# Kernel optimization log

Measured on AMD Instinct MI355X. Metric: run time of the kernel, lower is better.

The kernel has to match this reference:

```python
import jax, jax.numpy as jnp
import numpy as np

N, D, H = 8192, 256, 128


def setup_inputs() -> dict:
    key = jax.random.key(0)
    k1, k2, k3, k4 = jax.random.split(key, 4)
    x = jax.random.normal(k1, (N, D), dtype=jnp.float32)
    y = jax.random.normal(k2, (N, D), dtype=jnp.float32)
    W1 = jax.random.normal(k3, (D, H), dtype=jnp.float32) * (1.0 / np.sqrt(D))
    b1 = jnp.zeros((H,), dtype=jnp.float32)
    W2 = jax.random.normal(k4, (H, D), dtype=jnp.float32) * (1.0 / np.sqrt(H))
    b2 = jnp.zeros((D,), dtype=jnp.float32)
    return {"x": x, "y": y, "W1": W1, "b1": b1, "W2": W2, "b2": b2}


def _l2norm(v):
    # torch.nn.functional.normalize(dim=-1): v / max(||v||, eps)
    n = jnp.sqrt(jnp.sum(v * v, axis=-1, keepdims=True))
    return v / jnp.maximum(n, 1e-12)


def _neg_cos_loss_stopgrad(p, z):
    p_n = _l2norm(p)
    z_n = _l2norm(jax.lax.stop_gradient(z))
    return -jnp.mean(jnp.sum(p_n * z_n, axis=1))


def reference(x, y, W1, b1, W2, b2):
    def mlp(v):
        h = jax.nn.relu(v @ W1 + b1)
        return h @ W2 + b2

    p_x = mlp(x)
    p_y = mlp(y)
    loss = 0.5 * (_neg_cos_loss_stopgrad(p_x, y) + _neg_cos_loss_stopgrad(p_y, x))

    # accuracy branch (original naively broadcasts [N,D,1]*[1,D,N]; same math as matmul)
    p_x_n = _l2norm(p_x)
    p_y_n = _l2norm(p_y)
    x_n = _l2norm(x)
    y_n = _l2norm(y)
    sim_x = p_x_n @ y_n.T  # [N, N], sim_x[i, j] = p_x[i] . y[j]
    sim_y = p_y_n @ x_n.T  # [N, N]
    gold = jnp.arange(x.shape[0])
    # NOTE: faithful to original parenthesization: 0.5 * first term + second term
    acc_x = 0.5 * jnp.mean((jnp.argmax(sim_x, axis=0) == gold).astype(jnp.float32)) + \
            jnp.mean((jnp.argmax(sim_x, axis=1) == gold).astype(jnp.float32))
    acc_y = 0.5 * jnp.mean((jnp.argmax(sim_y, axis=0) == gold).astype(jnp.float32)) + \
            jnp.mean((jnp.argmax(sim_y, axis=1) == gold).astype(jnp.float32))
    return loss, acc_x, acc_y
```

## Files before the change

### kernel.cpp

```cpp
#include <hip/hip_runtime.h>


static constexpr int N = 8192;
static constexpr int D = 256;
static constexpr int H = 128;

typedef __attribute__((ext_vector_type(8))) short s16x8;
typedef __attribute__((ext_vector_type(4))) float fp32x4;
typedef unsigned long long ull;

__device__ __forceinline__ unsigned f2ord(float f) {
    unsigned u = __float_as_uint(f);
    return (u & 0x80000000u) ? ~u : (u | 0x80000000u);
}
__device__ __forceinline__ ull umax64(ull a, ull b) { return a > b ? a : b; }
__device__ __forceinline__ unsigned short bf16_rtne(float f) {
    unsigned u = __float_as_uint(f);
    unsigned r = 0x7FFFu + ((u >> 16) & 1u);
    return (unsigned short)((u + r) >> 16);
}
__device__ __forceinline__ float bf_f(unsigned short h) {
    return __uint_as_float((unsigned)h << 16);
}
__device__ __forceinline__ void split_store(float f, unsigned short* h, unsigned short* l) {
    unsigned short hb = bf16_rtne(f);
    *h = hb;
    *l = bf16_rtne(f - bf_f(hb));
}
__device__ __forceinline__ void gload16(const unsigned short* g, void* lds) {
    __builtin_amdgcn_global_load_lds(
        (const __attribute__((address_space(1))) unsigned int*)g,
        (__attribute__((address_space(3))) unsigned int*)lds, 16, 0, 0);
}
__device__ __forceinline__ size_t gidx(int panel, int kt, int kq, int m) {
    return (((size_t)(panel * 8 + kt) * 4 + kq) * 128 + m) * 8;
}

static constexpr int MLP_ROWS = 32;

__global__ __launch_bounds__(256) void prep_kernel(
    const float* __restrict__ x, const float* __restrict__ y,
    const float* __restrict__ W1, const float* __restrict__ b1,
    const float* __restrict__ W2, const float* __restrict__ b2,
    unsigned short* __restrict__ pxh, unsigned short* __restrict__ pxl,
    unsigned short* __restrict__ pyh, unsigned short* __restrict__ pyl,
    unsigned short* __restrict__ xh, unsigned short* __restrict__ xl,
    unsigned short* __restrict__ yh, unsigned short* __restrict__ yl,
    ull* __restrict__ keys, int* __restrict__ cnt, float* __restrict__ diagParts)
{
    const int bid = blockIdx.x;
    const int t = threadIdx.x;

    if (bid < 512) {
        __shared__ float sV[MLP_ROWS][D + 4];
        __shared__ float sH[MLP_ROWS][H + 4];
        __shared__ float sNrm[MLP_ROWS];

        const float* V = (bid < 256) ? x : y;
        unsigned short* Ph = (bid < 256) ? pxh : pyh;
        unsigned short* Pl = (bid < 256) ? pxl : pyl;
        const int rowBase = (bid & 255) * MLP_ROWS;

        for (int i = t; i < MLP_ROWS * (D / 4); i += 256) {
            int r = i >> 6, c4 = i & 63;
            float4 v = *reinterpret_cast<const float4*>(&V[(size_t)(rowBase + r) * D + c4 * 4]);
            sV[r][c4 * 4 + 0] = v.x; sV[r][c4 * 4 + 1] = v.y;
            sV[r][c4 * 4 + 2] = v.z; sV[r][c4 * 4 + 3] = v.w;
        }
        __syncthreads();

        {
            const int c = t & (H - 1);
            const int r0 = (t >> 7) * 16;
            float acc[16];
#pragma unroll
            for (int i = 0; i < 16; ++i) acc[i] = 0.f;
            for (int k4 = 0; k4 < D / 4; ++k4) {
                float w0 = W1[(k4 * 4 + 0) * H + c];
                float w1 = W1[(k4 * 4 + 1) * H + c];
                float w2 = W1[(k4 * 4 + 2) * H + c];
                float w3 = W1[(k4 * 4 + 3) * H + c];
#pragma unroll
                for (int i = 0; i < 16; ++i) {
                    float4 v = *reinterpret_cast<const float4*>(&sV[r0 + i][k4 * 4]);
                    acc[i] = fmaf(v.w, w3, fmaf(v.z, w2, fmaf(v.y, w1, fmaf(v.x, w0, acc[i]))));
                }
            }
            float bb = b1[c];
#pragma unroll
            for (int i = 0; i < 16; ++i) {
                float h = acc[i] + bb;
                sH[r0 + i][c] = h > 0.f ? h : 0.f;
            }
        }
        __syncthreads();

        {
            const int c = t;
            float acc[MLP_ROWS];
#pragma unroll
            for (int i = 0; i < MLP_ROWS; ++i) acc[i] = 0.f;
            for (int k4 = 0; k4 < H / 4; ++k4) {
                float w0 = W2[(k4 * 4 + 0) * D + c];
                float w1 = W2[(k4 * 4 + 1) * D + c];
                float w2 = W2[(k4 * 4 + 2) * D + c];
                float w3 = W2[(k4 * 4 + 3) * D + c];
#pragma unroll
                for (int i = 0; i < MLP_ROWS; ++i) {
                    float4 v = *reinterpret_cast<const float4*>(&sH[i][k4 * 4]);
                    acc[i] = fmaf(v.w, w3, fmaf(v.z, w2, fmaf(v.y, w1, fmaf(v.x, w0, acc[i]))));
                }
            }
            float bb = b2[c];
            __syncthreads();
#pragma unroll
            for (int i = 0; i < MLP_ROWS; ++i) sV[i][c] = acc[i] + bb;
        }
        __syncthreads();

        {
            const int wave = t >> 6, lane = t & 63;
            for (int r = wave; r < MLP_ROWS; r += 4) {
                float s = 0.f;
#pragma unroll
                for (int c = 0; c < D / 64; ++c) {
                    float v = sV[r][lane + c * 64];
                    s = fmaf(v, v, s);
                }
#pragma unroll
                for (int off = 32; off > 0; off >>= 1) s += __shfl_down(s, off);
                if (lane == 0) sNrm[r] = s;
            }
        }
        __syncthreads();

        for (int i = t; i < MLP_ROWS * (D / 4); i += 256) {
            int r = i >> 6, c4 = i & 63;
            float scale = 1.0f / fmaxf(sqrtf(sNrm[r]), 1e-12f);
            ushort4 h, l;
            split_store(sV[r][c4 * 4 + 0] * scale, &h.x, &l.x);
            split_store(sV[r][c4 * 4 + 1] * scale, &h.y, &l.y);
            split_store(sV[r][c4 * 4 + 2] * scale, &h.z, &l.z);
            split_store(sV[r][c4 * 4 + 3] * scale, &h.w, &l.w);
            int grow = rowBase + r;
            size_t g = gidx(grow >> 7, c4 >> 3, (c4 >> 1) & 3, grow & 127) + (size_t)(c4 & 1) * 4;
            *reinterpret_cast<ushort4*>(&Ph[g]) = h;
            *reinterpret_cast<ushort4*>(&Pl[g]) = l;
        }
    } else {
        const int rb = bid - 512;
        if (t < 128) keys[rb * 128 + t] = 0ULL;
        if (bid == 512) {
            if (t < 128) diagParts[t] = 0.f;
            if (t < 4) cnt[t] = 0;
        }
        const int wave = t >> 6, lane = t & 63;
#pragma unroll 1
        for (int i = 0; i < 16; ++i) {
            int gr = rb * 64 + wave * 16 + i;
            const float* V = (gr < N) ? x : y;
            unsigned short* Vh = (gr < N) ? xh : yh;
            unsigned short* Vl = (gr < N) ? xl : yl;
            int row = gr & (N - 1);
            float4 v = *reinterpret_cast<const float4*>(&V[(size_t)row * D + lane * 4]);
            float s = fmaf(v.x, v.x, fmaf(v.y, v.y, fmaf(v.z, v.z, v.w * v.w)));
#pragma unroll
            for (int off = 32; off > 0; off >>= 1) s += __shfl_down(s, off);
            s = __shfl(s, 0);
            float scale = 1.0f / fmaxf(sqrtf(s), 1e-12f);
            ushort4 h, l;
            split_store(v.x * scale, &h.x, &l.x);
            split_store(v.y * scale, &h.y, &l.y);
            split_store(v.z * scale, &h.z, &l.z);
            split_store(v.w * scale, &h.w, &l.w);
            size_t g = gidx(row >> 7, lane >> 3, (lane >> 1) & 3, row & 127) + (size_t)(lane & 1) * 4;
            *reinterpret_cast<ushort4*>(&Vh[g]) = h;
            *reinterpret_cast<ushort4*>(&Vl[g]) = l;
        }
    }
}

__global__ __launch_bounds__(256, 4) void sim_argmax_mfma(
    const unsigned short* __restrict__ Ah, const unsigned short* __restrict__ Al,
    const unsigned short* __restrict__ Bh, const unsigned short* __restrict__ Bl,
    ull* __restrict__ rowKeys, ull* __restrict__ colKeys,
    float* __restrict__ diagParts)
{
    __shared__ s16x8 sS[4][512];
    __shared__ ull kbufR[128][2];
    __shared__ ull kbufC[128][2];
    __shared__ float sDiag[4];

    const int t = threadIdx.x;
    const int w = t >> 6, lane = t & 63;
    const int wr = w >> 1, wc = w & 1;

    const int bid = blockIdx.x;
    const int xcd = bid & 7, local = bid >> 3;
    const int rowTile = (xcd & 3) * 16 + (local & 15);
    const int colTile = (xcd >> 2) * 32 + (local >> 4);
    const int rowBase = rowTile * 128;
    const int colBase = colTile * 128;

    fp32x4 acc[4][4];
#pragma unroll
    for (int i = 0; i < 4; ++i)
#pragma unroll
        for (int j = 0; j < 4; ++j) acc[i][j] = (fp32x4){0.f, 0.f, 0.f, 0.f};

    const unsigned short* pAh = Ah + (size_t)rowTile * 4096 * 8;
    const unsigned short* pAl = Al + (size_t)rowTile * 4096 * 8;
    const unsigned short* pBh = Bh + (size_t)colTile * 4096 * 8;
    const unsigned short* pBl = Bl + (size_t)colTile * 4096 * 8;

#define STAGE(kt)                                                               \
    do {                                                                        \
        const size_t o0 = (size_t)(kt) * 512 + w * 128 + lane;                  \
        const size_t o1 = o0 + 64;                                              \
        gload16(pAh + o0 * 8, (void*)&sS[0][w * 128]);                          \
        gload16(pAh + o1 * 8, (void*)&sS[0][w * 128 + 64]);                     \
        gload16(pAl + o0 * 8, (void*)&sS[1][w * 128]);                          \
        gload16(pAl + o1 * 8, (void*)&sS[1][w * 128 + 64]);                     \
        gload16(pBh + o0 * 8, (void*)&sS[2][w * 128]);                          \
        gload16(pBh + o1 * 8, (void*)&sS[2][w * 128 + 64]);                     \
        gload16(pBl + o0 * 8, (void*)&sS[3][w * 128]);                          \
        gload16(pBl + o1 * 8, (void*)&sS[3][w * 128 + 64]);                     \
    } while (0)

    STAGE(0);

    const int fBase = (lane >> 4) * 128 + (lane & 15);
    const int aBase = fBase + wr * 64;
    const int bBase = fBase + wc * 64;

#pragma unroll 1
    for (int kt = 0; kt < 8; ++kt) {
        __syncthreads();

        s16x8 ah[4], bh[4];
#pragma unroll
        for (int f = 0; f < 4; ++f) ah[f] = sS[0][aBase + f * 16];
#pragma unroll
        for (int f = 0; f < 4; ++f) bh[f] = sS[2][bBase + f * 16];
        __builtin_amdgcn_s_setprio(1);
#pragma unroll
        for (int fm = 0; fm < 4; ++fm)
#pragma unroll
            for (int fn = 0; fn < 4; ++fn)
                acc[fm][fn] = __builtin_amdgcn_mfma_f32_16x16x32_bf16(ah[fm], bh[fn], acc[fm][fn], 0, 0, 0);
        __builtin_amdgcn_s_setprio(0);

        {
            s16x8 al[4];
#pragma unroll
            for (int f = 0; f < 4; ++f) al[f] = sS[1][aBase + f * 16];
            __builtin_amdgcn_s_setprio(1);
#pragma unroll
            for (int fm = 0; fm < 4; ++fm)
#pragma unroll
                for (int fn = 0; fn < 4; ++fn)
                    acc[fm][fn] = __builtin_amdgcn_mfma_f32_16x16x32_bf16(al[fm], bh[fn], acc[fm][fn], 0, 0, 0);
            __builtin_amdgcn_s_setprio(0);
        }

        {
            s16x8 bl[4];
#pragma unroll
            for (int f = 0; f < 4; ++f) bl[f] = sS[3][bBase + f * 16];

            __syncthreads();
            if (kt < 7) STAGE(kt + 1);

            __builtin_amdgcn_s_setprio(1);
#pragma unroll
            for (int fm = 0; fm < 4; ++fm)
#pragma unroll
                for (int fn = 0; fn < 4; ++fn)
                    acc[fm][fn] = __builtin_amdgcn_mfma_f32_16x16x32_bf16(ah[fm], bl[fn], acc[fm][fn], 0, 0, 0);
            __builtin_amdgcn_s_setprio(0);
        }
    }
#undef STAGE

    const int R0 = wr * 64;
    const int C0 = wc * 64;

    if (rowTile == colTile) {
        float s = 0.f;
        if (wr == wc) {
            int dr = (lane & 15) - (lane >> 4) * 4;
            if (dr >= 0 && dr < 4) {
#pragma unroll
                for (int fm = 0; fm < 4; ++fm) s += acc[fm][fm][dr];
            }
        }
#pragma unroll
        for (int off = 32; off > 0; off >>= 1) s += __shfl_down(s, off);
        if (lane == 0) sDiag[w] = s;
        __syncthreads();
        if (t == 0) diagParts[rowTile] = ((sDiag[0] + sDiag[1]) + sDiag[2]) + sDiag[3];
    }

#pragma unroll
    for (int fm = 0; fm < 4; ++fm) {
#pragma unroll
        for (int r = 0; r < 4; ++r) {
            int rowLoc = R0 + fm * 16 + (lane >> 4) * 4 + r;
            float m = fmaxf(fmaxf(acc[fm][0][r], acc[fm][1][r]), fmaxf(acc[fm][2][r], acc[fm][3][r]));
#pragma unroll
            for (int off = 1; off < 16; off <<= 1) m = fmaxf(m, __shfl_xor(m, off));
            unsigned idx = 0xFFFFFFFFu;
#pragma unroll
            for (int fn = 0; fn < 4; ++fn) {
                unsigned gcol = (unsigned)(colBase + C0 + fn * 16 + (lane & 15));
                if (acc[fm][fn][r] == m && gcol < idx) idx = gcol;
            }
#pragma unroll
            for (int off = 1; off < 16; off <<= 1) {
                unsigned o = __shfl_xor(idx, off);
                if (o < idx) idx = o;
            }
            if ((lane & 15) == 0)
                kbufR[rowLoc][wc] = ((ull)f2ord(m) << 32) | (unsigned)(~idx);
        }
    }

#pragma unroll
    for (int fn = 0; fn < 4; ++fn) {
        int colLoc = C0 + fn * 16 + (lane & 15);
        float m = -3.4e38f;
#pragma unroll
        for (int fm = 0; fm < 4; ++fm) {
            float m01 = fmaxf(acc[fm][fn][0], acc[fm][fn][1]);
            float m23 = fmaxf(acc[fm][fn][2], acc[fm][fn][3]);
            m = fmaxf(m, fmaxf(m01, m23));
        }
        m = fmaxf(m, __shfl_xor(m, 16));
        m = fmaxf(m, __shfl_xor(m, 32));
        unsigned idx = 0xFFFFFFFFu;
#pragma unroll
        for (int fm = 0; fm < 4; ++fm) {
#pragma unroll
            for (int r = 0; r < 4; ++r) {
                unsigned grow = (unsigned)(rowBase + R0 + fm * 16 + (lane >> 4) * 4 + r);
                if (acc[fm][fn][r] == m && grow < idx) idx = grow;
            }
        }
        {
            unsigned o = __shfl_xor(idx, 16);
            if (o < idx) idx = o;
            o = __shfl_xor(idx, 32);
            if (o < idx) idx = o;
        }
        if ((lane >> 4) == 0)
            kbufC[colLoc][wr] = ((ull)f2ord(m) << 32) | (unsigned)(~idx);
    }

    __syncthreads();

    if (t < 128) {
        ull best = umax64(kbufR[t][0], kbufR[t][1]);
        atomicMax(&rowKeys[rowBase + t], best);
    } else {
        int c = t - 128;
        ull best = umax64(kbufC[c][0], kbufC[c][1]);
        atomicMax(&colKeys[colBase + c], best);
    }
}

__global__ __launch_bounds__(256) void count_kernel(const ull* __restrict__ keys, int* __restrict__ cnt)
{
    const int t = threadIdx.x;
    const int i = blockIdx.x * 256 + t;
    const int lane = t & 63;
#pragma unroll
    for (int a = 0; a < 4; ++a) {
        int s = ((~(unsigned)keys[a * N + i]) == (unsigned)i);
#pragma unroll
        for (int off = 32; off > 0; off >>= 1) s += __shfl_down(s, off);
        if (lane == 0) atomicAdd(&cnt[a], s);
    }
}

__global__ __launch_bounds__(64) void final_kernel(
    const float* __restrict__ diagParts, const int* __restrict__ cnt, float* __restrict__ out)
{
    const int lane = threadIdx.x;
    double vx = (double)diagParts[lane];
    double vy = (double)diagParts[64 + lane];
#pragma unroll
    for (int off = 32; off > 0; off >>= 1) {
        vx += __shfl_down(vx, off);
        vy += __shfl_down(vy, off);
    }
    if (lane == 0) {
        float invN = 1.0f / (float)N;
        out[0] = (float)(-0.5 * (vx + vy) / (double)N);
        out[1] = 0.5f * ((float)cnt[1] * invN) + (float)cnt[0] * invN;
        out[2] = 0.5f * ((float)cnt[3] * invN) + (float)cnt[2] * invN;
    }
}

extern "C" void kernel_launch(void* const* d_in, const int* in_sizes, int n_in,
                              void* d_out, int out_size, void* d_ws, size_t ws_size,
                              hipStream_t stream)
{
    (void)in_sizes; (void)n_in; (void)out_size; (void)ws_size;
    const float* x  = (const float*)d_in[0];
    const float* y  = (const float*)d_in[1];
    const float* W1 = (const float*)d_in[2];
    const float* b1 = (const float*)d_in[3];
    const float* W2 = (const float*)d_in[4];
    const float* b2 = (const float*)d_in[5];
    float* out = (float*)d_out;

    const size_t ND = (size_t)N * D;
    unsigned short* pxh = (unsigned short*)d_ws;
    unsigned short* pxl = pxh + ND;
    unsigned short* pyh = pxl + ND;
    unsigned short* pyl = pyh + ND;
    unsigned short* xh  = pyl + ND;
    unsigned short* xl  = xh + ND;
    unsigned short* yh  = xl + ND;
    unsigned short* yl  = yh + ND;
    ull* keys = (ull*)(yl + ND);
    ull* rkx = keys + 0 * N;
    ull* ckx = keys + 1 * N;
    ull* rky = keys + 2 * N;
    ull* cky = keys + 3 * N;
    float* diagParts = (float*)(keys + 4 * N);
    int* cnt = (int*)(diagParts + 128);

    prep_kernel<<<768, 256, 0, stream>>>(x, y, W1, b1, W2, b2,
                                         pxh, pxl, pyh, pyl, xh, xl, yh, yl,
                                         keys, cnt, diagParts);

    sim_argmax_mfma<<<4096, 256, 0, stream>>>(pxh, pxl, yh, yl, rkx, ckx, diagParts);
    sim_argmax_mfma<<<4096, 256, 0, stream>>>(pyh, pyl, xh, xl, rky, cky, diagParts + 64);

    count_kernel<<<32, 256, 0, stream>>>(keys, cnt);
    final_kernel<<<1, 64, 0, stream>>>(diagParts, cnt, out);
}
```

Measured before the change: 323.7 us.

## Merge both similarity kernels into one launch and move next-stage load after MFMAs

The two sim_argmax_mfma launches (p_x vs y and p_y vs x) become a single 8192-block grid, where the high bit of blockIdx picks which pair of operands and output slots to use. This removes one launch and its tail drain between the two GEMMs. The barrier and STAGE prefetch of the next k-tile also move from before the third MFMA group to after it. That removes a barrier from the middle of the compute, but the global-to-LDS load may overlap less with the MFMAs, which can expose load latency.

```diff
diff --git a/kernel.cpp b/kernel.cpp
--- a/kernel.cpp
+++ b/kernel.cpp
@@ -181,10 +181,11 @@
 }
 
 __global__ __launch_bounds__(256, 4) void sim_argmax_mfma(
-    const unsigned short* __restrict__ Ah, const unsigned short* __restrict__ Al,
-    const unsigned short* __restrict__ Bh, const unsigned short* __restrict__ Bl,
-    ull* __restrict__ rowKeys, ull* __restrict__ colKeys,
-    float* __restrict__ diagParts)
+    const unsigned short* __restrict__ Axh, const unsigned short* __restrict__ Axl,
+    const unsigned short* __restrict__ Byh, const unsigned short* __restrict__ Byl,
+    const unsigned short* __restrict__ Ayh, const unsigned short* __restrict__ Ayl,
+    const unsigned short* __restrict__ Bxh, const unsigned short* __restrict__ Bxl,
+    ull* __restrict__ keys, float* __restrict__ diagParts)
 {
     __shared__ s16x8 sS[4][512];
     __shared__ ull kbufR[128][2];
@@ -195,7 +196,18 @@
     const int w = t >> 6, lane = t & 63;
     const int wr = w >> 1, wc = w & 1;
 
-    const int bid = blockIdx.x;
+    const int bidFull = blockIdx.x;
+    const int sim = bidFull >> 12;
+    const int bid = bidFull & 4095;
+
+    const unsigned short* Ah = sim ? Ayh : Axh;
+    const unsigned short* Al = sim ? Ayl : Axl;
+    const unsigned short* Bh = sim ? Bxh : Byh;
+    const unsigned short* Bl = sim ? Bxl : Byl;
+    ull* rowKeys = keys + (sim ? 2 * N : 0);
+    ull* colKeys = keys + (sim ? 3 * N : (size_t)N);
+    float* diagP = diagParts + (sim ? 64 : 0);
+
     const int xcd = bid & 7, local = bid >> 3;
     const int rowTile = (xcd & 3) * 16 + (local & 15);
     const int colTile = (xcd >> 2) * 32 + (local >> 4);
@@ -262,15 +274,10 @@
                     acc[fm][fn] = __builtin_amdgcn_mfma_f32_16x16x32_bf16(al[fm], bh[fn], acc[fm][fn], 0, 0, 0);
             __builtin_amdgcn_s_setprio(0);
         }
-
         {
             s16x8 bl[4];
 #pragma unroll
             for (int f = 0; f < 4; ++f) bl[f] = sS[3][bBase + f * 16];
-
-            __syncthreads();
-            if (kt < 7) STAGE(kt + 1);
-
             __builtin_amdgcn_s_setprio(1);
 #pragma unroll
             for (int fm = 0; fm < 4; ++fm)
@@ -279,6 +286,9 @@
                     acc[fm][fn] = __builtin_amdgcn_mfma_f32_16x16x32_bf16(ah[fm], bl[fn], acc[fm][fn], 0, 0, 0);
             __builtin_amdgcn_s_setprio(0);
         }
+
+        __syncthreads();
+        if (kt < 7) STAGE(kt + 1);
     }
 #undef STAGE
 
@@ -298,7 +308,7 @@
         for (int off = 32; off > 0; off >>= 1) s += __shfl_down(s, off);
         if (lane == 0) sDiag[w] = s;
         __syncthreads();
-        if (t == 0) diagParts[rowTile] = ((sDiag[0] + sDiag[1]) + sDiag[2]) + sDiag[3];
+        if (t == 0) diagP[rowTile] = ((sDiag[0] + sDiag[1]) + sDiag[2]) + sDiag[3];
     }
 
 #pragma unroll
@@ -424,10 +434,6 @@
     unsigned short* yh  = xl + ND;
     unsigned short* yl  = yh + ND;
     ull* keys = (ull*)(yl + ND);
-    ull* rkx = keys + 0 * N;
-    ull* ckx = keys + 1 * N;
-    ull* rky = keys + 2 * N;
-    ull* cky = keys + 3 * N;
     float* diagParts = (float*)(keys + 4 * N);
     int* cnt = (int*)(diagParts + 128);
 
@@ -435,8 +441,9 @@
                                          pxh, pxl, pyh, pyl, xh, xl, yh, yl,
                                          keys, cnt, diagParts);
 
-    sim_argmax_mfma<<<4096, 256, 0, stream>>>(pxh, pxl, yh, yl, rkx, ckx, diagParts);
-    sim_argmax_mfma<<<4096, 256, 0, stream>>>(pyh, pyl, xh, xl, rky, cky, diagParts + 64);
+    sim_argmax_mfma<<<8192, 256, 0, stream>>>(pxh, pxl, yh, yl,
+                                              pyh, pyl, xh, xl,
+                                              keys, diagParts);
 
     count_kernel<<<32, 256, 0, stream>>>(keys, cnt);
     final_kernel<<<1, 64, 0, stream>>>(diagParts, cnt, out);
```

New measurement: 283.5 us. 12.4% less time.
